# Kernel optimization log

Hardware: AMD Instinct MI355X
Metric: run time of the kernel (lower is better)

Reference implementation:

```python
import jax, jax.numpy as jnp
import numpy as np

D_IN = 1024
D_OUT = 1024
NUM_HEADS = 16
HEAD_DIM = D_OUT // NUM_HEADS


def setup_inputs() -> dict:
    key = jax.random.key(0)
    ks = jax.random.split(key, 6)
    s = 0.02
    x = jax.random.normal(ks[0], (4, 2048, D_IN), dtype=jnp.float32)
    # nn.Linear weights are [out, in]
    Wq = jax.random.normal(ks[1], (D_OUT, D_IN), dtype=jnp.float32) * s
    Wk = jax.random.normal(ks[2], (D_OUT, D_IN), dtype=jnp.float32) * s
    Wv = jax.random.normal(ks[3], (D_OUT, D_IN), dtype=jnp.float32) * s
    Wo = jax.random.normal(ks[4], (D_OUT, D_OUT), dtype=jnp.float32) * s
    bo = jax.random.normal(ks[5], (D_OUT,), dtype=jnp.float32) * s
    return {"x": x, "Wq": Wq, "Wk": Wk, "Wv": Wv, "Wo": Wo, "bo": bo}


def reference(x, Wq, Wk, Wv, Wo, bo):
    B, T, _ = x.shape
    # project and split heads: [B, H, T, hd]
    def proj(W):
        return (x @ W.T).reshape(B, T, NUM_HEADS, HEAD_DIM).transpose(0, 2, 1, 3)
    q, k, v = proj(Wq), proj(Wk), proj(Wv)
    scores = jnp.einsum('bhqd,bhkd->bhqk', q, k) / jnp.sqrt(jnp.float32(HEAD_DIM))
    causal = jnp.tril(jnp.ones((T, T), dtype=bool))  # True = keep
    scores = jnp.where(causal, scores, -jnp.inf)
    attn = jax.nn.softmax(scores, axis=-1)
    ctx = jnp.einsum('bhqk,bhkd->bhqd', attn, v)  # [B,H,T,hd]
    ctx = ctx.transpose(0, 2, 1, 3).reshape(B, T, D_OUT)
    return ctx @ Wo.T + bo
```

## Files before the change

kernel.cpp:

```cpp
#include <hip/hip_runtime.h>

#define NH 16
#define HD 64
#define TSEQ 2048
#define DMODEL 1024

typedef __attribute__((ext_vector_type(8))) short short8;
typedef __attribute__((ext_vector_type(4))) float f32x4;

static __device__ __forceinline__ unsigned short f2bf(float f) {
    unsigned u = __builtin_bit_cast(unsigned, f);
    u += 0x7FFF + ((u >> 16) & 1);
    return (unsigned short)(u >> 16);
}

static __device__ __forceinline__ unsigned cvtpk(float a, float b) {
    unsigned r;
    asm("v_cvt_pk_bf16_f32 %0, %1, %2" : "=v"(r) : "v"(a), "v"(b));
    return r;
}

__global__ __launch_bounds__(256) void cast_f32_bf16(const float* __restrict__ src,
                                                     unsigned short* __restrict__ dst, int n4) {
    int i = blockIdx.x * 256 + threadIdx.x;
    if (i >= n4) return;
    float4 v = reinterpret_cast<const float4*>(src)[i];
    ushort4 o;
    o.x = f2bf(v.x); o.y = f2bf(v.y); o.z = f2bf(v.z); o.w = f2bf(v.w);
    reinterpret_cast<ushort4*>(dst)[i] = o;
}

__global__ __launch_bounds__(256) void cast_weights(const float* __restrict__ Wq,
                                                    const float* __restrict__ Wk,
                                                    const float* __restrict__ Wv,
                                                    const float* __restrict__ Wo,
                                                    unsigned short* __restrict__ dq,
                                                    unsigned short* __restrict__ dk,
                                                    unsigned short* __restrict__ dv,
                                                    unsigned short* __restrict__ dwo) {
    int g = blockIdx.x >> 10;
    int i = (blockIdx.x & 1023) * 256 + threadIdx.x;
    const float* s = (g == 0) ? Wq : (g == 1) ? Wk : (g == 2) ? Wv : Wo;
    unsigned short* d = (g == 0) ? dq : (g == 1) ? dk : (g == 2) ? dv : dwo;
    float4 v = reinterpret_cast<const float4*>(s)[i];
    ushort4 o;
    o.x = f2bf(v.x); o.y = f2bf(v.y); o.z = f2bf(v.z); o.w = f2bf(v.w);
    reinterpret_cast<ushort4*>(d)[i] = o;
}

static __device__ __forceinline__ void gemm_mainloop(const unsigned short* __restrict__ A,
                                                     const unsigned short* __restrict__ Bt,
                                                     int m0, int n0, int K,
                                                     unsigned short* As, unsigned short* Bs,
                                                     f32x4 acc[4][4]) {
    const int tid = threadIdx.x;
    const int lane = tid & 63;
    const int w = tid >> 6;
    const int wr = w >> 1, wc = w & 1;
    const int lrow = lane >> 2;
    const int lcol = (lane & 3) * 8;

    f32x4 zero = {0.f, 0.f, 0.f, 0.f};
#pragma unroll
    for (int i = 0; i < 4; i++)
#pragma unroll
        for (int j = 0; j < 4; j++) acc[i][j] = zero;

    auto stage = [&](int k0, int buf) {
#pragma unroll
        for (int c = w; c < 8; c += 4) {
            int row = c * 16 + lrow;
            __builtin_amdgcn_global_load_lds(
                (const __attribute__((address_space(1))) void*)(A + (size_t)(m0 + row) * K + k0 + lcol),
                (__attribute__((address_space(3))) void*)(As + buf * 4096 + c * 512), 16, 0, 0);
            __builtin_amdgcn_global_load_lds(
                (const __attribute__((address_space(1))) void*)(Bt + (size_t)(n0 + row) * K + k0 + lcol),
                (__attribute__((address_space(3))) void*)(Bs + buf * 4096 + c * 512), 16, 0, 0);
        }
    };

    stage(0, 0);
    __syncthreads();
    int cur = 0;
    for (int k0 = 0; k0 < K; k0 += 32) {
        if (k0 + 32 < K) stage(k0 + 32, cur ^ 1);
        const unsigned short* Ab = As + cur * 4096;
        const unsigned short* Bb = Bs + cur * 4096;
        const int ko = (lane >> 4) * 8;
        short8 a[4], b[4];
#pragma unroll
        for (int i = 0; i < 4; i++)
            a[i] = *(const short8*)(Ab + (wr * 64 + i * 16 + (lane & 15)) * 32 + ko);
#pragma unroll
        for (int j = 0; j < 4; j++)
            b[j] = *(const short8*)(Bb + (wc * 64 + j * 16 + (lane & 15)) * 32 + ko);
#pragma unroll
        for (int i = 0; i < 4; i++)
#pragma unroll
            for (int j = 0; j < 4; j++)
                acc[i][j] = __builtin_amdgcn_mfma_f32_16x16x32_bf16(a[i], b[j], acc[i][j], 0, 0, 0);
        __syncthreads();
        cur ^= 1;
    }
}

#define QSCALE 0.180336880f
__global__ __launch_bounds__(256) void gemm_qkv(const unsigned short* __restrict__ xb,
                                                const unsigned short* __restrict__ Wqb,
                                                const unsigned short* __restrict__ Wkb,
                                                const unsigned short* __restrict__ Wvb,
                                                unsigned short* __restrict__ Q,
                                                unsigned short* __restrict__ K,
                                                unsigned short* __restrict__ Vt) {
    __shared__ __attribute__((aligned(16))) unsigned short As[2 * 128 * 32];
    __shared__ __attribute__((aligned(16))) unsigned short Bs[2 * 128 * 32];
    const int m0 = blockIdx.x * 128;
    const int n0 = blockIdx.y * 128;
    const int z = blockIdx.z;
    const unsigned short* Bt = (z == 0) ? Wqb : ((z == 1) ? Wkb : Wvb);
    unsigned short* out = (z == 0) ? Q : ((z == 1) ? K : Vt);

    f32x4 acc[4][4];
    gemm_mainloop(xb, Bt, m0, n0, DMODEL, As, Bs, acc);

    const int tid = threadIdx.x, lane = tid & 63, w = tid >> 6;
    const int wr = w >> 1, wc = w & 1;
    const float sc = (z == 0) ? QSCALE : 1.0f;
#pragma unroll
    for (int i = 0; i < 4; i++)
#pragma unroll
        for (int j = 0; j < 4; j++)
#pragma unroll
            for (int r = 0; r < 4; r++) {
                int row = m0 + wr * 64 + i * 16 + (lane >> 4) * 4 + r;
                int col = n0 + wc * 64 + j * 16 + (lane & 15);
                int b = row >> 11, t = row & 2047;
                int h = col >> 6, d = col & 63;
                unsigned short v = f2bf(acc[i][j][r] * sc);
                if (z == 2)
                    out[(((size_t)(b * NH + h)) * HD + d) * TSEQ + t] = v;
                else
                    out[(((size_t)(b * NH + h)) * TSEQ + t) * HD + d] = v;
            }
}

__global__ __launch_bounds__(256) void gemm_out(const unsigned short* __restrict__ ctx,
                                                const unsigned short* __restrict__ Wob,
                                                const float* __restrict__ bo,
                                                float* __restrict__ out) {
    __shared__ __attribute__((aligned(16))) unsigned short As[2 * 128 * 32];
    __shared__ __attribute__((aligned(16))) unsigned short Bs[2 * 128 * 32];
    const int m0 = blockIdx.x * 128;
    const int n0 = blockIdx.y * 128;

    f32x4 acc[4][4];
    gemm_mainloop(ctx, Wob, m0, n0, DMODEL, As, Bs, acc);

    const int tid = threadIdx.x, lane = tid & 63, w = tid >> 6;
    const int wr = w >> 1, wc = w & 1;
#pragma unroll
    for (int i = 0; i < 4; i++)
#pragma unroll
        for (int j = 0; j < 4; j++)
#pragma unroll
            for (int r = 0; r < 4; r++) {
                int row = m0 + wr * 64 + i * 16 + (lane >> 4) * 4 + r;
                int col = n0 + wc * 64 + j * 16 + (lane & 15);
                out[(size_t)row * DMODEL + col] = acc[i][j][r] + bo[col];
            }
}

__global__ __launch_bounds__(256) void attn(const unsigned short* __restrict__ Qg,
                                            const unsigned short* __restrict__ Kg,
                                            const unsigned short* __restrict__ Vg,
                                            unsigned short* __restrict__ ctx) {
    __shared__ __attribute__((aligned(16))) unsigned short Ks[64][72];
    __shared__ __attribute__((aligned(16))) unsigned short Vs[64][72];
    __shared__ __attribute__((aligned(16))) unsigned short Pl[128][76];

    const int tid = threadIdx.x, lane = tid & 63, w = tid >> 6;
    const int wq = w * 32;
    const int lg = lane >> 4;
    const int ll = lane & 15;
    const int bh = blockIdx.x;
    const int q0 = (gridDim.y - 1 - blockIdx.y) * 128;
    const unsigned short* Qh = Qg + (size_t)bh * TSEQ * HD;
    const unsigned short* Kh = Kg + (size_t)bh * TSEQ * HD;
    const unsigned short* Vh = Vg + (size_t)bh * HD * TSEQ;

    short8 qf[2][2];
#pragma unroll
    for (int rb = 0; rb < 2; rb++)
#pragma unroll
        for (int ks = 0; ks < 2; ks++)
            qf[rb][ks] = *(const short8*)(Qh + (size_t)(q0 + wq + rb * 16 + ll) * HD + ks * 32 + lg * 8);

    float mrun[2] = {-1e30f, -1e30f}, lrun[2] = {0.f, 0.f};
    const f32x4 zerov = {0.f, 0.f, 0.f, 0.f};
    f32x4 o_t[2][4];
#pragma unroll
    for (int rb = 0; rb < 2; rb++)
#pragma unroll
        for (int db = 0; db < 4; db++) o_t[rb][db] = zerov;

    const int sr = tid >> 3;
    const int sc = (tid & 7) * 8;
    short8 kreg0, kreg1, vreg0, vreg1;
    {
        kreg0 = *(const short8*)(Kh + (size_t)(sr) * HD + sc);
        kreg1 = *(const short8*)(Kh + (size_t)(sr + 32) * HD + sc);
        vreg0 = *(const short8*)(Vh + (size_t)sr * TSEQ + sc);
        vreg1 = *(const short8*)(Vh + (size_t)(sr + 32) * TSEQ + sc);
    }

    const int nkv = q0 / 64 + 2;
    for (int kt = 0; kt < nkv; kt++) {
        const int kv0 = kt * 64;
        __builtin_amdgcn_s_barrier();
        __builtin_amdgcn_sched_barrier(0);
        *(short8*)&Ks[sr][sc] = kreg0;
        *(short8*)&Ks[sr + 32][sc] = kreg1;
        *(short8*)&Vs[sr][sc] = vreg0;
        *(short8*)&Vs[sr + 32][sc] = vreg1;
        if (kt + 1 < nkv) {
            const int nv0 = kv0 + 64;
            kreg0 = *(const short8*)(Kh + (size_t)(nv0 + sr) * HD + sc);
            kreg1 = *(const short8*)(Kh + (size_t)(nv0 + sr + 32) * HD + sc);
            vreg0 = *(const short8*)(Vh + (size_t)sr * TSEQ + nv0 + sc);
            vreg1 = *(const short8*)(Vh + (size_t)(sr + 32) * TSEQ + nv0 + sc);
        }
        __builtin_amdgcn_sched_barrier(0);
        asm volatile("s_waitcnt lgkmcnt(0)" ::: "memory");
        __builtin_amdgcn_s_barrier();
        __builtin_amdgcn_sched_barrier(0);

        short8 af0[4], af1[4];
#pragma unroll
        for (int cb = 0; cb < 4; cb++) {
            af0[cb] = *(const short8*)&Ks[cb * 16 + ll][lg * 8];
            af1[cb] = *(const short8*)&Ks[cb * 16 + ll][32 + lg * 8];
        }
        f32x4 st[2][4];
#pragma unroll
        for (int rb = 0; rb < 2; rb++)
#pragma unroll
            for (int cb = 0; cb < 4; cb++)
                st[rb][cb] = __builtin_amdgcn_mfma_f32_16x16x32_bf16(af0[cb], qf[rb][0], zerov, 0, 0, 0);
#pragma unroll
        for (int rb = 0; rb < 2; rb++)
#pragma unroll
            for (int cb = 0; cb < 4; cb++)
                st[rb][cb] = __builtin_amdgcn_mfma_f32_16x16x32_bf16(af1[cb], qf[rb][1], st[rb][cb], 0, 0, 0);

        if (kv0 + 63 > q0) {
#pragma unroll
            for (int rb = 0; rb < 2; rb++)
#pragma unroll
                for (int cb = 0; cb < 4; cb++)
#pragma unroll
                    for (int r = 0; r < 4; r++) {
                        int kvl = cb * 16 + lg * 4 + r;
                        int ql = wq + rb * 16 + ll;
                        if (kv0 + kvl > q0 + ql) st[rb][cb][r] = -1e30f;
                    }
        }

        float mx[2];
#pragma unroll
        for (int rb = 0; rb < 2; rb++) {
            float a0 = fmaxf(fmaxf(st[rb][0][0], st[rb][0][1]), fmaxf(st[rb][0][2], st[rb][0][3]));
            float a1 = fmaxf(fmaxf(st[rb][1][0], st[rb][1][1]), fmaxf(st[rb][1][2], st[rb][1][3]));
            float a2 = fmaxf(fmaxf(st[rb][2][0], st[rb][2][1]), fmaxf(st[rb][2][2], st[rb][2][3]));
            float a3 = fmaxf(fmaxf(st[rb][3][0], st[rb][3][1]), fmaxf(st[rb][3][2], st[rb][3][3]));
            float m = fmaxf(fmaxf(a0, a1), fmaxf(a2, a3));
            m = fmaxf(m, __shfl_xor(m, 16));
            m = fmaxf(m, __shfl_xor(m, 32));
            mx[rb] = m;
        }
        float need = fmaxf(mx[0] - mrun[0], mx[1] - mrun[1]);
        if (__any(need > 8.f)) {
#pragma unroll
            for (int rb = 0; rb < 2; rb++) {
                float mold = mrun[rb];
                float mn = fmaxf(mold, mx[rb]);
                float rs = __builtin_amdgcn_exp2f(mold - mn);
                mrun[rb] = mn;
                lrun[rb] *= rs;
#pragma unroll
                for (int db = 0; db < 4; db++)
#pragma unroll
                    for (int r = 0; r < 4; r++) o_t[rb][db][r] *= rs;
            }
        }
#pragma unroll
        for (int rb = 0; rb < 2; rb++) {
            float sum = 0.f;
#pragma unroll
            for (int cb = 0; cb < 4; cb++) {
                float p0 = __builtin_amdgcn_exp2f(st[rb][cb][0] - mrun[rb]);
                float p1 = __builtin_amdgcn_exp2f(st[rb][cb][1] - mrun[rb]);
                float p2 = __builtin_amdgcn_exp2f(st[rb][cb][2] - mrun[rb]);
                float p3 = __builtin_amdgcn_exp2f(st[rb][cb][3] - mrun[rb]);
                sum += (p0 + p1) + (p2 + p3);
                uint2 pw;
                pw.x = cvtpk(p0, p1);
                pw.y = cvtpk(p2, p3);
                *(uint2*)&Pl[wq + rb * 16 + ll][cb * 16 + lg * 4] = pw;
            }
            sum += __shfl_xor(sum, 16);
            sum += __shfl_xor(sum, 32);
            lrun[rb] += sum;
        }
        asm volatile("s_waitcnt lgkmcnt(0)" ::: "memory");
        __builtin_amdgcn_sched_barrier(0);

#pragma unroll
        for (int ks = 0; ks < 2; ks++) {
            short8 pa[2], va[4];
#pragma unroll
            for (int rb = 0; rb < 2; rb++)
                pa[rb] = *(const short8*)&Pl[wq + rb * 16 + ll][ks * 32 + lg * 8];
#pragma unroll
            for (int db = 0; db < 4; db++)
                va[db] = *(const short8*)&Vs[db * 16 + ll][ks * 32 + lg * 8];
#pragma unroll
            for (int rb = 0; rb < 2; rb++)
#pragma unroll
                for (int db = 0; db < 4; db++)
                    o_t[rb][db] = __builtin_amdgcn_mfma_f32_16x16x32_bf16(va[db], pa[rb], o_t[rb][db], 0, 0, 0);
        }
    }

    const int b = bh >> 4, h = bh & 15;
#pragma unroll
    for (int rb = 0; rb < 2; rb++) {
        float linv = 1.f / lrun[rb];
#pragma unroll
        for (int db = 0; db < 4; db++) {
            uint2 pw;
            pw.x = cvtpk(o_t[rb][db][0] * linv, o_t[rb][db][1] * linv);
            pw.y = cvtpk(o_t[rb][db][2] * linv, o_t[rb][db][3] * linv);
            *(uint2*)&Pl[wq + rb * 16 + ll][db * 16 + lg * 4] = pw;
        }
    }
    asm volatile("s_waitcnt lgkmcnt(0)" ::: "memory");
    __builtin_amdgcn_sched_barrier(0);
#pragma unroll
    for (int rb = 0; rb < 2; rb++)
#pragma unroll
        for (int half = 0; half < 2; half++) {
            short8 v = *(const short8*)&Pl[wq + rb * 16 + ll][half * 32 + lg * 8];
            size_t row = (size_t)(b * TSEQ + q0 + wq + rb * 16 + ll);
            *(short8*)(ctx + (row * NH + h) * HD + half * 32 + lg * 8) = v;
        }
}

extern "C" void kernel_launch(void* const* d_in, const int* in_sizes, int n_in,
                              void* d_out, int out_size, void* d_ws, size_t ws_size,
                              hipStream_t stream) {
    const float* x  = (const float*)d_in[0];
    const float* Wq = (const float*)d_in[1];
    const float* Wk = (const float*)d_in[2];
    const float* Wv = (const float*)d_in[3];
    const float* Wo = (const float*)d_in[4];
    const float* bo = (const float*)d_in[5];
    float* out = (float*)d_out;

    char* ws = (char*)d_ws;
    unsigned short* xb   = (unsigned short*)(ws);
    unsigned short* Wqb  = (unsigned short*)(ws + 16777216);
    unsigned short* Wkb  = (unsigned short*)(ws + 18874368);
    unsigned short* Wvb  = (unsigned short*)(ws + 20971520);
    unsigned short* Wob  = (unsigned short*)(ws + 23068672);
    unsigned short* Qb   = (unsigned short*)(ws + 25165824);
    unsigned short* Kb   = (unsigned short*)(ws + 41943040);
    unsigned short* Vtb  = (unsigned short*)(ws + 58720256);
    unsigned short* ctxb = (unsigned short*)(ws + 75497472);

    cast_f32_bf16<<<8192, 256, 0, stream>>>(x, xb, 2097152);
    cast_weights<<<4096, 256, 0, stream>>>(Wq, Wk, Wv, Wo, Wqb, Wkb, Wvb, Wob);

    gemm_qkv<<<dim3(64, 8, 3), 256, 0, stream>>>(xb, Wqb, Wkb, Wvb, Qb, Kb, Vtb);
    attn<<<dim3(64, 16), 256, 0, stream>>>(Qb, Kb, Vtb, ctxb);
    gemm_out<<<dim3(64, 8), 256, 0, stream>>>(ctxb, Wob, bo, out);
}
```

Measured before the change: 198.4 us.

## Rewrite GEMM mainloop with 256x128 tiles, 8 waves and staggered multi-buffer prefetch

Replaces the 128x128 double-buffered GEMM mainloop used by the QKV and output projections. The new one uses 256x128 tiles, 512 threads, and a K-step of 64. A tiles are double-buffered and B tiles triple-buffered. The global-to-LDS loads are split into quarter stages interleaved with MFMA phases under explicit barriers, setprio and waitcnt. LDS columns are XOR-swizzled to avoid bank conflicts, which is meant to raise MFMA utilisation and hide load latency. The cost is much larger LDS use, fewer blocks, and a fragile hand-scheduled sync pattern.

```diff
diff --git a/kernel.cpp b/kernel.cpp
--- a/kernel.cpp
+++ b/kernel.cpp
@@ -48,92 +48,184 @@
     reinterpret_cast<ushort4*>(d)[i] = o;
 }
 
-static __device__ __forceinline__ void gemm_mainloop(const unsigned short* __restrict__ A,
-                                                     const unsigned short* __restrict__ Bt,
-                                                     int m0, int n0, int K,
-                                                     unsigned short* As, unsigned short* Bs,
-                                                     f32x4 acc[4][4]) {
-    const int tid = threadIdx.x;
-    const int lane = tid & 63;
-    const int w = tid >> 6;
-    const int wr = w >> 1, wc = w & 1;
-    const int lrow = lane >> 2;
-    const int lcol = (lane & 3) * 8;
-
-    f32x4 zero = {0.f, 0.f, 0.f, 0.f};
-#pragma unroll
-    for (int i = 0; i < 4; i++)
-#pragma unroll
-        for (int j = 0; j < 4; j++) acc[i][j] = zero;
-
-    auto stage = [&](int k0, int buf) {
-#pragma unroll
-        for (int c = w; c < 8; c += 4) {
-            int row = c * 16 + lrow;
+static __device__ __forceinline__ void gemm256_mainloop(
+    const unsigned short* __restrict__ A, const unsigned short* __restrict__ Bt,
+    int m0, int n0, unsigned short* As, unsigned short* Bs, f32x4 acc[8][2]) {
+    const int tid = threadIdx.x, lane = tid & 63, w = tid >> 6;
+    const int wr = w >> 2, wc = w & 3;
+    const int lg = lane >> 4, ll = lane & 15;
+    const int srow = tid >> 3;
+    const int scol8 = (tid & 7) * 8;
+
+    const f32x4 zero = {0.f, 0.f, 0.f, 0.f};
+#pragma unroll
+    for (int i = 0; i < 8; i++)
+#pragma unroll
+        for (int j = 0; j < 2; j++) acc[i][j] = zero;
+
+    auto stageA2 = [&](int kt, int buf, int h) {
+#pragma unroll
+        for (int s = h * 2; s < h * 2 + 2; ++s) {
+            int row = s * 64 + srow;
+            int csw = scol8 ^ (((row >> 2) & 1) << 4);
             __builtin_amdgcn_global_load_lds(
-                (const __attribute__((address_space(1))) void*)(A + (size_t)(m0 + row) * K + k0 + lcol),
-                (__attribute__((address_space(3))) void*)(As + buf * 4096 + c * 512), 16, 0, 0);
-            __builtin_amdgcn_global_load_lds(
-                (const __attribute__((address_space(1))) void*)(Bt + (size_t)(n0 + row) * K + k0 + lcol),
-                (__attribute__((address_space(3))) void*)(Bs + buf * 4096 + c * 512), 16, 0, 0);
+                (const __attribute__((address_space(1))) void*)(A + (size_t)(m0 + row) * DMODEL + kt * 64 + csw),
+                (__attribute__((address_space(3))) void*)(As + buf * 16384 + s * 4096 + w * 512), 16, 0, 0);
         }
     };
-
-    stage(0, 0);
-    __syncthreads();
-    int cur = 0;
-    for (int k0 = 0; k0 < K; k0 += 32) {
-        if (k0 + 32 < K) stage(k0 + 32, cur ^ 1);
-        const unsigned short* Ab = As + cur * 4096;
-        const unsigned short* Bb = Bs + cur * 4096;
-        const int ko = (lane >> 4) * 8;
-        short8 a[4], b[4];
-#pragma unroll
-        for (int i = 0; i < 4; i++)
-            a[i] = *(const short8*)(Ab + (wr * 64 + i * 16 + (lane & 15)) * 32 + ko);
-#pragma unroll
-        for (int j = 0; j < 4; j++)
-            b[j] = *(const short8*)(Bb + (wc * 64 + j * 16 + (lane & 15)) * 32 + ko);
-#pragma unroll
-        for (int i = 0; i < 4; i++)
-#pragma unroll
-            for (int j = 0; j < 4; j++)
-                acc[i][j] = __builtin_amdgcn_mfma_f32_16x16x32_bf16(a[i], b[j], acc[i][j], 0, 0, 0);
-        __syncthreads();
-        cur ^= 1;
+    auto stageB1 = [&](int kt, int buf, int s) {
+        int row = s * 64 + srow;
+        int csw = scol8 ^ (((row >> 2) & 1) << 4);
+        __builtin_amdgcn_global_load_lds(
+            (const __attribute__((address_space(1))) void*)(Bt + (size_t)(n0 + row) * DMODEL + kt * 64 + csw),
+            (__attribute__((address_space(3))) void*)(Bs + buf * 8192 + s * 4096 + w * 512), 16, 0, 0);
+    };
+    auto ldA = [&](int buf, int row, int ks) -> short8 {
+        int col = (ks * 32 + lg * 8) ^ (((row >> 2) & 1) << 4);
+        return *(const short8*)(As + buf * 16384 + row * 64 + col);
+    };
+    auto ldB = [&](int buf, int row, int ks) -> short8 {
+        int col = (ks * 32 + lg * 8) ^ (((row >> 2) & 1) << 4);
+        return *(const short8*)(Bs + buf * 8192 + row * 64 + col);
+    };
+
+    stageA2(0, 0, 0); stageA2(0, 0, 1);
+    stageB1(0, 0, 0); stageB1(0, 0, 1);
+    stageB1(1, 1, 0); stageB1(1, 1, 1);
+    asm volatile("s_waitcnt vmcnt(2)" ::: "memory");
+    __builtin_amdgcn_s_barrier();
+    __builtin_amdgcn_sched_barrier(0);
+
+#pragma unroll 1
+    for (int kt = 0; kt < 16; ++kt) {
+        const int pa = kt & 1;
+        const int pb = kt % 3;
+        short8 bfr[2][2];
+        short8 afr[2][2];
+
+#pragma unroll
+        for (int j = 0; j < 2; j++)
+#pragma unroll
+            for (int ks = 0; ks < 2; ks++)
+                bfr[j][ks] = ldB(pb, wc * 32 + j * 16 + ll, ks);
+#pragma unroll
+        for (int i2 = 0; i2 < 2; i2++)
+#pragma unroll
+            for (int ks = 0; ks < 2; ks++)
+                afr[i2][ks] = ldA(pa, wr * 128 + i2 * 16 + ll, ks);
+        if (kt + 1 < 16) stageA2(kt + 1, pa ^ 1, 0);
+        __builtin_amdgcn_s_barrier();
+        __builtin_amdgcn_sched_barrier(0);
+        __builtin_amdgcn_s_setprio(1);
+#pragma unroll
+        for (int i2 = 0; i2 < 2; i2++)
+#pragma unroll
+            for (int j = 0; j < 2; j++) {
+                acc[i2][j] = __builtin_amdgcn_mfma_f32_16x16x32_bf16(afr[i2][0], bfr[j][0], acc[i2][j], 0, 0, 0);
+                acc[i2][j] = __builtin_amdgcn_mfma_f32_16x16x32_bf16(afr[i2][1], bfr[j][1], acc[i2][j], 0, 0, 0);
+            }
+        __builtin_amdgcn_s_setprio(0);
+        __builtin_amdgcn_s_barrier();
+        __builtin_amdgcn_sched_barrier(0);
+
+#pragma unroll
+        for (int i2 = 0; i2 < 2; i2++)
+#pragma unroll
+            for (int ks = 0; ks < 2; ks++)
+                afr[i2][ks] = ldA(pa, wr * 128 + (2 + i2) * 16 + ll, ks);
+        if (kt + 1 < 16) stageA2(kt + 1, pa ^ 1, 1);
+        __builtin_amdgcn_s_barrier();
+        __builtin_amdgcn_sched_barrier(0);
+        __builtin_amdgcn_s_setprio(1);
+#pragma unroll
+        for (int i2 = 0; i2 < 2; i2++)
+#pragma unroll
+            for (int j = 0; j < 2; j++) {
+                acc[2 + i2][j] = __builtin_amdgcn_mfma_f32_16x16x32_bf16(afr[i2][0], bfr[j][0], acc[2 + i2][j], 0, 0, 0);
+                acc[2 + i2][j] = __builtin_amdgcn_mfma_f32_16x16x32_bf16(afr[i2][1], bfr[j][1], acc[2 + i2][j], 0, 0, 0);
+            }
+        __builtin_amdgcn_s_setprio(0);
+        __builtin_amdgcn_s_barrier();
+        __builtin_amdgcn_sched_barrier(0);
+
+#pragma unroll
+        for (int i2 = 0; i2 < 2; i2++)
+#pragma unroll
+            for (int ks = 0; ks < 2; ks++)
+                afr[i2][ks] = ldA(pa, wr * 128 + (4 + i2) * 16 + ll, ks);
+        if (kt + 2 < 16) stageB1(kt + 2, (kt + 2) % 3, 0);
+        __builtin_amdgcn_s_barrier();
+        __builtin_amdgcn_sched_barrier(0);
+        __builtin_amdgcn_s_setprio(1);
+#pragma unroll
+        for (int i2 = 0; i2 < 2; i2++)
+#pragma unroll
+            for (int j = 0; j < 2; j++) {
+                acc[4 + i2][j] = __builtin_amdgcn_mfma_f32_16x16x32_bf16(afr[i2][0], bfr[j][0], acc[4 + i2][j], 0, 0, 0);
+                acc[4 + i2][j] = __builtin_amdgcn_mfma_f32_16x16x32_bf16(afr[i2][1], bfr[j][1], acc[4 + i2][j], 0, 0, 0);
+            }
+        __builtin_amdgcn_s_setprio(0);
+        __builtin_amdgcn_s_barrier();
+        __builtin_amdgcn_sched_barrier(0);
+
+#pragma unroll
+        for (int i2 = 0; i2 < 2; i2++)
+#pragma unroll
+            for (int ks = 0; ks < 2; ks++)
+                afr[i2][ks] = ldA(pa, wr * 128 + (6 + i2) * 16 + ll, ks);
+        if (kt + 2 < 16) {
+            stageB1(kt + 2, (kt + 2) % 3, 1);
+            asm volatile("s_waitcnt vmcnt(2)" ::: "memory");
+        } else {
+            asm volatile("s_waitcnt vmcnt(0)" ::: "memory");
+        }
+        __builtin_amdgcn_s_barrier();
+        __builtin_amdgcn_sched_barrier(0);
+        __builtin_amdgcn_s_setprio(1);
+#pragma unroll
+        for (int i2 = 0; i2 < 2; i2++)
+#pragma unroll
+            for (int j = 0; j < 2; j++) {
+                acc[6 + i2][j] = __builtin_amdgcn_mfma_f32_16x16x32_bf16(afr[i2][0], bfr[j][0], acc[6 + i2][j], 0, 0, 0);
+                acc[6 + i2][j] = __builtin_amdgcn_mfma_f32_16x16x32_bf16(afr[i2][1], bfr[j][1], acc[6 + i2][j], 0, 0, 0);
+            }
+        __builtin_amdgcn_s_setprio(0);
+        __builtin_amdgcn_s_barrier();
+        __builtin_amdgcn_sched_barrier(0);
     }
 }
 
 #define QSCALE 0.180336880f
-__global__ __launch_bounds__(256) void gemm_qkv(const unsigned short* __restrict__ xb,
+__global__ __launch_bounds__(512) void gemm_qkv(const unsigned short* __restrict__ xb,
                                                 const unsigned short* __restrict__ Wqb,
                                                 const unsigned short* __restrict__ Wkb,
                                                 const unsigned short* __restrict__ Wvb,
                                                 unsigned short* __restrict__ Q,
                                                 unsigned short* __restrict__ K,
                                                 unsigned short* __restrict__ Vt) {
-    __shared__ __attribute__((aligned(16))) unsigned short As[2 * 128 * 32];
-    __shared__ __attribute__((aligned(16))) unsigned short Bs[2 * 128 * 32];
-    const int m0 = blockIdx.x * 128;
+    __shared__ __attribute__((aligned(16))) unsigned short As[2 * 256 * 64];
+    __shared__ __attribute__((aligned(16))) unsigned short Bs[3 * 128 * 64];
+    const int m0 = blockIdx.x * 256;
     const int n0 = blockIdx.y * 128;
     const int z = blockIdx.z;
     const unsigned short* Bt = (z == 0) ? Wqb : ((z == 1) ? Wkb : Wvb);
     unsigned short* out = (z == 0) ? Q : ((z == 1) ? K : Vt);
 
-    f32x4 acc[4][4];
-    gemm_mainloop(xb, Bt, m0, n0, DMODEL, As, Bs, acc);
-
-    const int tid = threadIdx.x, lane = tid & 63, w = tid >> 6;
-    const int wr = w >> 1, wc = w & 1;
+    f32x4 acc[8][2];
+    gemm256_mainloop(xb, Bt, m0, n0, As, Bs, acc);
+
+    const int lane = threadIdx.x & 63, w = threadIdx.x >> 6;
+    const int wr = w >> 2, wc = w & 3;
+    const int lg = lane >> 4, ll = lane & 15;
     const float sc = (z == 0) ? QSCALE : 1.0f;
 #pragma unroll
-    for (int i = 0; i < 4; i++)
-#pragma unroll
-        for (int j = 0; j < 4; j++)
+    for (int i = 0; i < 8; i++)
+#pragma unroll
+        for (int j = 0; j < 2; j++)
 #pragma unroll
             for (int r = 0; r < 4; r++) {
-                int row = m0 + wr * 64 + i * 16 + (lane >> 4) * 4 + r;
-                int col = n0 + wc * 64 + j * 16 + (lane & 15);
+                int row = m0 + wr * 128 + i * 16 + lg * 4 + r;
+                int col = n0 + wc * 32 + j * 16 + ll;
                 int b = row >> 11, t = row & 2047;
                 int h = col >> 6, d = col & 63;
                 unsigned short v = f2bf(acc[i][j][r] * sc);
@@ -144,30 +236,33 @@
             }
 }
 
-__global__ __launch_bounds__(256) void gemm_out(const unsigned short* __restrict__ ctx,
+__global__ __launch_bounds__(512) void gemm_out(const unsigned short* __restrict__ ctx,
                                                 const unsigned short* __restrict__ Wob,
                                                 const float* __restrict__ bo,
                                                 float* __restrict__ out) {
-    __shared__ __attribute__((aligned(16))) unsigned short As[2 * 128 * 32];
-    __shared__ __attribute__((aligned(16))) unsigned short Bs[2 * 128 * 32];
-    const int m0 = blockIdx.x * 128;
+    __shared__ __attribute__((aligned(16))) unsigned short As[2 * 256 * 64];
+    __shared__ __attribute__((aligned(16))) unsigned short Bs[3 * 128 * 64];
+    const int m0 = blockIdx.x * 256;
     const int n0 = blockIdx.y * 128;
 
-    f32x4 acc[4][4];
-    gemm_mainloop(ctx, Wob, m0, n0, DMODEL, As, Bs, acc);
-
-    const int tid = threadIdx.x, lane = tid & 63, w = tid >> 6;
-    const int wr = w >> 1, wc = w & 1;
-#pragma unroll
-    for (int i = 0; i < 4; i++)
-#pragma unroll
-        for (int j = 0; j < 4; j++)
+    f32x4 acc[8][2];
+    gemm256_mainloop(ctx, Wob, m0, n0, As, Bs, acc);
+
+    const int lane = threadIdx.x & 63, w = threadIdx.x >> 6;
+    const int wr = w >> 2, wc = w & 3;
+    const int lg = lane >> 4, ll = lane & 15;
+#pragma unroll
+    for (int i = 0; i < 8; i++)
+#pragma unroll
+        for (int j = 0; j < 2; j++) {
+            int col = n0 + wc * 32 + j * 16 + ll;
+            float bias = bo[col];
 #pragma unroll
             for (int r = 0; r < 4; r++) {
-                int row = m0 + wr * 64 + i * 16 + (lane >> 4) * 4 + r;
-                int col = n0 + wc * 64 + j * 16 + (lane & 15);
-                out[(size_t)row * DMODEL + col] = acc[i][j][r] + bo[col];
-            }
+                int row = m0 + wr * 128 + i * 16 + lg * 4 + r;
+                out[(size_t)row * DMODEL + col] = acc[i][j][r] + bias;
+            }
+        }
 }
 
 __global__ __launch_bounds__(256) void attn(const unsigned short* __restrict__ Qg,
@@ -380,7 +475,7 @@
     cast_f32_bf16<<<8192, 256, 0, stream>>>(x, xb, 2097152);
     cast_weights<<<4096, 256, 0, stream>>>(Wq, Wk, Wv, Wo, Wqb, Wkb, Wvb, Wob);
 
-    gemm_qkv<<<dim3(64, 8, 3), 256, 0, stream>>>(xb, Wqb, Wkb, Wvb, Qb, Kb, Vtb);
+    gemm_qkv<<<dim3(32, 8, 3), 512, 0, stream>>>(xb, Wqb, Wkb, Wvb, Qb, Kb, Vtb);
     attn<<<dim3(64, 16), 256, 0, stream>>>(Qb, Kb, Vtb, ctxb);
-    gemm_out<<<dim3(64, 8), 256, 0, stream>>>(ctxb, Wob, bo, out);
-}
+    gemm_out<<<dim3(32, 8), 512, 0, stream>>>(ctxb, Wob, bo, out);
+}
```

New measurement: 207.8 us. +4.7%, slower.
